# Performance work log

Measured on AMD Instinct MI355X. Metric: run time of the kernel, lower is better.

## Reference

```python
import jax, jax.numpy as jnp
import numpy as np

LN_EPS = 1e-5

def _gru_layer(x, W_ih, W_hh, b_ih, b_hh):
    # x: [B,S,Din]; W_ih: [3H,Din]; W_hh: [3H,H]; biases: [3H]
    B = x.shape[0]
    H = W_hh.shape[1]
    # Precompute input-side gate projections for all timesteps (one big GEMM).
    gx = jnp.einsum('bsd,gd->bsg', x, W_ih) + b_ih  # [B,S,3H]
    Whh_T = W_hh.T  # [H,3H]

    def step(h, gx_t):
        gh = h @ Whh_T + b_hh                     # [B,3H]
        xr, xz, xn = jnp.split(gx_t, 3, axis=-1)
        hr, hz, hn = jnp.split(gh, 3, axis=-1)
        r = jax.nn.sigmoid(xr + hr)
        z = jax.nn.sigmoid(xz + hz)
        n = jnp.tanh(xn + r * hn)
        h_new = (1.0 - z) * n + z * h
        return h_new, h_new

    h0 = jnp.zeros((B, H), dtype=x.dtype)
    h_last, ys = jax.lax.scan(step, h0, jnp.swapaxes(gx, 0, 1))  # ys: [S,B,H]
    return jnp.swapaxes(ys, 0, 1), h_last


def setup_inputs() -> dict:
    key = jax.random.key(0)
    ks = jax.random.split(key, 12)
    B, S, D, H = 256, 512, 64, 256
    L = 3
    s_in = 1.0 / np.sqrt(H)
    return {
        'x': jax.random.normal(ks[0], (B, S, D), dtype=jnp.float32),
        'W_ih0': jax.random.uniform(ks[1], (3 * H, D), jnp.float32, -s_in, s_in),
        'W_ih_rest': jax.random.uniform(ks[2], (L - 1, 3 * H, H), jnp.float32, -s_in, s_in),
        'W_hh': jax.random.uniform(ks[3], (L, 3 * H, H), jnp.float32, -s_in, s_in),
        'b_ih': jax.random.uniform(ks[4], (L, 3 * H), jnp.float32, -s_in, s_in),
        'b_hh': jax.random.uniform(ks[5], (L, 3 * H), jnp.float32, -s_in, s_in),
        'ln_gamma': jnp.ones((H,), jnp.float32),
        'ln_beta': jnp.zeros((H,), jnp.float32),
        'W1': jax.random.uniform(ks[6], (32, H), jnp.float32, -s_in, s_in),
        'b1': jax.random.uniform(ks[7], (32,), jnp.float32, -s_in, s_in),
        'W2': jax.random.uniform(ks[8], (1, 32), jnp.float32, -1 / np.sqrt(32), 1 / np.sqrt(32)),
        'b2': jax.random.uniform(ks[9], (1,), jnp.float32, -1 / np.sqrt(32), 1 / np.sqrt(32)),
    }


def reference(x, W_ih0, W_ih_rest, W_hh, b_ih, b_hh, ln_gamma, ln_beta, W1, b1, W2, b2):
    # Multi-layer GRU (batch_first), eval mode (dropout inactive).
    h = x
    L = W_hh.shape[0]
    h_last = None
    for l in range(L):
        W_ih_l = W_ih0 if l == 0 else W_ih_rest[l - 1]
        h, h_last = _gru_layer(h, W_ih_l, W_hh[l], b_ih[l], b_hh[l])
    last = h_last  # == out[:, -1, :]  [B,H]
    # LayerNorm
    mu = jnp.mean(last, axis=-1, keepdims=True)
    var = jnp.mean(jnp.square(last - mu), axis=-1, keepdims=True)
    last = (last - mu) * jax.lax.rsqrt(var + LN_EPS) * ln_gamma + ln_beta
    # MLP head
    hdn = jax.nn.relu(last @ W1.T + b1)
    pred = hdn @ W2.T + b2  # [B,1]
    return pred[:, 0]
```

## Files before the change

kernel.cpp:

```cpp
#include <hip/hip_runtime.h>
#include <stdint.h>

#define B_  256
#define S_  512
#define D_  64
#define H_  256
#define G3_ 768

typedef __attribute__((ext_vector_type(8))) short s8v;
typedef __attribute__((ext_vector_type(4))) short s4v;
typedef __attribute__((ext_vector_type(4))) float f4v;
typedef __attribute__((ext_vector_type(4))) float f4r;

#define MF(a, b, c) __builtin_amdgcn_mfma_f32_16x16x32_bf16((a), (b), (c), 0, 0, 0)

__device__ __forceinline__ unsigned short f2bf(float x) {
  unsigned u = __float_as_uint(x);
  unsigned r = (u + 0x7fffu + ((u >> 16) & 1u)) >> 16;
  return (unsigned short)r;
}
__device__ __forceinline__ float sigm(float x) {
  return __builtin_amdgcn_rcpf(1.f + __expf(-x));
}
__device__ __forceinline__ float tanh_f(float x) {
  return 1.f - 2.f * __builtin_amdgcn_rcpf(1.f + __expf(2.f * x));
}

__global__ __launch_bounds__(256) void pack_bf16(
    const float* __restrict__ src, unsigned short* __restrict__ dst, int n8)
{
  const int i = blockIdx.x * 256 + threadIdx.x;
  if (i >= n8) return;
  const float4 f0 = *(const float4*)(src + (size_t)i * 8);
  const float4 f1 = *(const float4*)(src + (size_t)i * 8 + 4);
  unsigned short h[8] = { f2bf(f0.x), f2bf(f0.y), f2bf(f0.z), f2bf(f0.w),
                          f2bf(f1.x), f2bf(f1.y), f2bf(f1.z), f2bf(f1.w) };
  *(s8v*)&dst[(size_t)i * 8] = *(s8v*)h;
}

__global__ __launch_bounds__(64) void pack_whh(
    const float* __restrict__ Whh, unsigned short* __restrict__ Whp,
    const float* __restrict__ bih, const float* __restrict__ bhh,
    float* __restrict__ bias2)
{
  const int gti = blockIdx.x, kc = blockIdx.y, lane = threadIdx.x;
  const int rowp = gti * 16 + (lane & 15);
  const int k0  = kc * 32 + (lane >> 4) * 8;
  const float* src = &Whh[(size_t)rowp * H_ + k0];
  unsigned short hi8[8];
  #pragma unroll
  for (int s = 0; s < 8; ++s) hi8[s] = f2bf(src[s]);
  const size_t o = ((size_t)(gti * 8 + kc) * 64 + lane) * 8;
  *(s8v*)&Whp[o] = *(s8v*)hi8;

  if (gti == 0 && kc == 0) {
    #pragma unroll
    for (int i = 0; i < 12; ++i) {
      int g = i * 64 + lane;
      bias2[g] = bih[g] + (g < 512 ? bhh[g] : 0.f);
    }
  }
}

__global__ __launch_bounds__(1024, 4) void fused_step(
    int s, int CH, int chsh, int cpl,
    const float* __restrict__ x, unsigned short* __restrict__ ybf,
    const unsigned short* __restrict__ wihp,
    const unsigned short* __restrict__ Whp, const float* __restrict__ bhh_all,
    const float* __restrict__ bias2, float* __restrict__ gxbase,
    float* __restrict__ hbuf)
{
  const int tid = threadIdx.x;
  const int wid = tid >> 6, lane = tid & 63;
  const int fr = lane & 15, fq = lane >> 4;
  const size_t gx_elems = (size_t)B_ * CH * G3_;

  extern __shared__ unsigned short lds_[];

  if (blockIdx.x < 48) {
    const int l = blockIdx.x >> 4;
    const int c = s - 2 * l;
    if (c < 0 || c >= cpl) return;

    const unsigned short* Whp_s = Whp + (size_t)l * G3_ * H_;
    const float* bhh_s = bhh_all + (size_t)l * G3_;
    float* hb = hbuf + (size_t)l * B_ * H_;
    const float* gx_r = gxbase + (size_t)(2 * l + (c & 1)) * gx_elems;
    const int t0s = c * CH;
    const int lastL = (l == 2) ? 1 : 0;

    unsigned short* WhN  = lds_;
    unsigned short* Abuf = lds_ + 65536;

    const int bid = blockIdx.x & 15;
    const int b0  = bid * 16;
    const int bb  = fr;

    const s8v* WhpV = (const s8v*)Whp_s;

    s8v whr[8], whz[8];
    #pragma unroll
    for (int kc = 0; kc < 8; ++kc) {
      whr[kc] = WhpV[((     wid) * 8 + kc) * 64 + lane];
      whz[kc] = WhpV[((16 + wid) * 8 + kc) * 64 + lane];
    }
    #pragma unroll
    for (int kc = 0; kc < 8; ++kc) {
      s8v v = WhpV[((32 + wid) * 8 + kc) * 64 + lane];
      *(s8v*)&WhN[(wid * 8 + kc) * 512 + lane * 8] = v;
    }

    const int u0 = 16 * wid + 4 * fq;
    const f4r bhn4 = *(const f4r*)&bhh_s[2 * H_ + u0];

    f4r hn4 = {0.f, 0.f, 0.f, 0.f};
    if (t0s != 0) hn4 = *(const f4r*)&hb[(size_t)(b0 + bb) * H_ + u0];

    const int kcw  = wid >> 1;
    const int lp   = bb | (((2 * wid + (fq >> 1)) & 3) << 4);
    const int eo   = (fq & 1) * 4;
    const int aoff = kcw * 512 + lp * 8 + eo;

    {
      s4v hh;
      #pragma unroll
      for (int j = 0; j < 4; ++j) hh[j] = (short)f2bf(hn4[j]);
      *(s4v*)&Abuf[aoff] = hh;
    }

    const float* gb0 = gx_r + ((size_t)(b0 + bb) * CH) * G3_;
    f4r xr4 = *(const f4r*)(gb0 + u0);
    f4r xz4 = *(const f4r*)(gb0 + H_ + u0);
    f4r xn4 = *(const f4r*)(gb0 + 2 * H_ + u0);

    int cur = 0;
    for (int t = 0; t < CH; ++t) {
      __syncthreads();

      const int tn = (t + 1 < CH) ? t + 1 : t;
      const float* gbn = gx_r + ((size_t)(b0 + bb) * CH + tn) * G3_;
      f4r xr_n = *(const f4r*)(gbn + u0);
      f4r xz_n = *(const f4r*)(gbn + H_ + u0);
      f4r xn_n = *(const f4r*)(gbn + 2 * H_ + u0);

      f4v accR = {}, accZ = {}, accN = {};
      #pragma unroll
      for (int kc = 0; kc < 8; ++kc) {
        s8v ahh = *(const s8v*)&Abuf[cur * 4096 + kc * 512 + lane * 8];
        s8v wn  = *(const s8v*)&WhN[(wid * 8 + kc) * 512 + lane * 8];
        accR = MF(whr[kc], ahh, accR);
        accZ = MF(whz[kc], ahh, accZ);
        accN = MF(wn,      ahh, accN);
      }

      #pragma unroll
      for (int i = 0; i < 4; ++i) {
        const float r = sigm(xr4[i] + accR[i]);
        const float z = sigm(xz4[i] + accZ[i]);
        const float n = tanh_f(xn4[i] + r * (accN[i] + bhn4[i]));
        hn4[i] = (1.f - z) * n + z * hn4[i];
      }
      s4v hh;
      #pragma unroll
      for (int j = 0; j < 4; ++j) hh[j] = (short)f2bf(hn4[j]);
      if (!lastL) {
        __builtin_nontemporal_store(
            hh, (s4v*)&ybf[((size_t)(b0 + bb) * S_ + (t0s + t)) * H_ + u0]);
      }
      *(s4v*)&Abuf[(cur ^ 1) * 4096 + aoff] = hh;
      xr4 = xr_n; xz4 = xz_n; xn4 = xn_n;
      cur ^= 1;
    }

    *(f4r*)&hb[(size_t)(b0 + bb) * H_ + u0] = hn4;

  } else {
    const int g = blockIdx.x - 48;
    const int per = CH * 12;
    const int l = g / per;
    if (l >= 3) return;
    const int c2 = s + 1 - 2 * l;
    if (c2 < 0 || c2 >= cpl) return;

    const int gidx  = g % per;
    const int mtile = gidx / 12, gtile = gidx % 12;
    const int r0 = mtile * 256, g0 = gtile * 64;

    const int    K   = (l == 0) ? D_ : H_;
    const unsigned short* Wp =
        (l == 0) ? wihp : (wihp + 49152 + (size_t)(l - 1) * 196608);
    const float* b2g = bias2 + l * 768;
    float* gx_w = gxbase + (size_t)(2 * l + (c2 & 1)) * gx_elems;
    const int t0g = c2 * CH;

    const int row = 16 * wid + fr;
    const int r = r0 + row;
    const int rg = ((r >> chsh) * S_) + t0g + (r & (CH - 1));

    const unsigned short* wp0 = Wp + (size_t)(g0 + fr) * K + fq * 8;

    f4v acc[4] = {};

    if (l == 0) {
      const float* apf = x + (size_t)rg * D_ + fq * 8;
      #pragma unroll
      for (int k0 = 0; k0 < D_; k0 += 32) {
        float4 f0 = *(const float4*)(apf + k0);
        float4 f1 = *(const float4*)(apf + k0 + 4);
        unsigned short a8[8] = { f2bf(f0.x), f2bf(f0.y), f2bf(f0.z), f2bf(f0.w),
                                 f2bf(f1.x), f2bf(f1.y), f2bf(f1.z), f2bf(f1.w) };
        s8v a = *(s8v*)a8;
        #pragma unroll
        for (int c = 0; c < 4; ++c) {
          s8v b = *(const s8v*)(wp0 + (size_t)c * 16 * K + k0);
          acc[c] = MF(a, b, acc[c]);
        }
      }
    } else {
      const unsigned short* ap = ybf + (size_t)rg * H_ + fq * 8;
      #pragma unroll
      for (int k0 = 0; k0 < H_; k0 += 32) {
        s8v a = *(const s8v*)(ap + k0);
        #pragma unroll
        for (int c = 0; c < 4; ++c) {
          s8v b = *(const s8v*)(wp0 + (size_t)c * 16 * K + k0);
          acc[c] = MF(a, b, acc[c]);
        }
      }
    }

    const int orow = r0 + wid * 16 + fq * 4;
    #pragma unroll
    for (int c = 0; c < 4; ++c) {
      const float bi = b2g[g0 + c * 16 + fr];
      #pragma unroll
      for (int i = 0; i < 4; ++i) {
        gx_w[(size_t)(orow + i) * G3_ + g0 + c * 16 + fr] = acc[c][i] + bi;
      }
    }
  }
}

__global__ __launch_bounds__(64) void head_kernel(
    const float* __restrict__ hlast, const float* __restrict__ lng,
    const float* __restrict__ lnb, const float* __restrict__ W1,
    const float* __restrict__ b1, const float* __restrict__ W2,
    const float* __restrict__ b2, float* __restrict__ out)
{
  const int b = blockIdx.x;
  const int lane = threadIdx.x;
  float4 v = *(const float4*)&hlast[(size_t)b * H_ + lane * 4];
  float s = v.x + v.y + v.z + v.w;
  #pragma unroll
  for (int m = 32; m > 0; m >>= 1) s += __shfl_xor(s, m, 64);
  const float mu = s * (1.f / 256.f);
  const float dx = v.x - mu, dy = v.y - mu, dz = v.z - mu, dw = v.w - mu;
  float q = dx*dx + dy*dy + dz*dz + dw*dw;
  #pragma unroll
  for (int m = 32; m > 0; m >>= 1) q += __shfl_xor(q, m, 64);
  const float rstd = rsqrtf(q * (1.f / 256.f) + 1e-5f);

  __shared__ float ln[256];
  const int i4 = lane * 4;
  ln[i4 + 0] = dx * rstd * lng[i4 + 0] + lnb[i4 + 0];
  ln[i4 + 1] = dy * rstd * lng[i4 + 1] + lnb[i4 + 1];
  ln[i4 + 2] = dz * rstd * lng[i4 + 2] + lnb[i4 + 2];
  ln[i4 + 3] = dw * rstd * lng[i4 + 3] + lnb[i4 + 3];
  __syncthreads();

  float hd = 0.f;
  if (lane < 32) {
    const float* w = W1 + (size_t)lane * H_;
    float a = 0.f;
    for (int k = 0; k < H_; ++k) a += ln[k] * w[k];
    a += b1[lane];
    hd = fmaxf(a, 0.f) * W2[lane];
  }
  #pragma unroll
  for (int m = 16; m > 0; m >>= 1) hd += __shfl_xor(hd, m, 64);
  if (lane == 0) out[b] = hd + b2[0];
}

extern "C" void kernel_launch(void* const* d_in, const int* in_sizes, int n_in,
                              void* d_out, int out_size, void* d_ws, size_t ws_size,
                              hipStream_t stream)
{
  const float* x     = (const float*)d_in[0];
  const float* W_ih0 = (const float*)d_in[1];
  const float* W_ihr = (const float*)d_in[2];
  const float* W_hh  = (const float*)d_in[3];
  const float* b_ih  = (const float*)d_in[4];
  const float* b_hh  = (const float*)d_in[5];
  const float* lng   = (const float*)d_in[6];
  const float* lnb   = (const float*)d_in[7];
  const float* W1    = (const float*)d_in[8];
  const float* b1    = (const float*)d_in[9];
  const float* W2    = (const float*)d_in[10];
  const float* b2    = (const float*)d_in[11];
  float* out = (float*)d_out;

  const size_t ybf_elems  = (size_t)B_ * S_ * H_;
  const size_t wihp_elems = 49152 + 2 * 196608;
  const size_t h_elems    = (size_t)B_ * H_;
  const size_t whp_elems  = (size_t)G3_ * H_;

  int CH = 32;
  while (CH > 8) {
    size_t need = ybf_elems * 2 + wihp_elems * 2
                + (6 * (size_t)B_ * CH * G3_ + 3 * h_elems + 3 * 768) * 4
                + 3 * whp_elems * 2 + 8192;
    if (need <= ws_size) break;
    CH >>= 1;
  }
  const int chsh = __builtin_ctz((unsigned)CH);
  const size_t gx_elems = (size_t)B_ * CH * G3_;
  const int cpl = S_ / CH;

  unsigned short* ybf  = (unsigned short*)d_ws;
  unsigned short* wihp = ybf + ybf_elems;
  float* gxbase = (float*)(wihp + wihp_elems);
  float* hbuf   = gxbase + 6 * gx_elems;
  unsigned short* Whp = (unsigned short*)(hbuf + 3 * h_elems);
  float* bias2 = (float*)(Whp + 3 * whp_elems);

  const size_t lds_bytes = 131072 + 16384;
  const int grid = 48 + 3 * CH * 12;

  pack_bf16<<<(49152 / 8 + 255) / 256, 256, 0, stream>>>(W_ih0, wihp, 49152 / 8);
  pack_bf16<<<(393216 / 8 + 255) / 256, 256, 0, stream>>>(
      W_ihr, wihp + 49152, 393216 / 8);
  for (int l = 0; l < 3; ++l) {
    pack_whh<<<dim3(48, 8), 64, 0, stream>>>(
        W_hh + (size_t)l * G3_ * H_, Whp + (size_t)l * whp_elems,
        b_ih + (size_t)l * G3_, b_hh + (size_t)l * G3_, bias2 + l * 768);
  }

  for (int s = -1; s <= cpl + 3; ++s) {
    fused_step<<<grid, 1024, lds_bytes, stream>>>(
        s, CH, chsh, cpl, x, ybf, wihp, Whp, b_hh, bias2, gxbase, hbuf);
  }

  head_kernel<<<256, 64, 0, stream>>>(hbuf + 2 * h_elems, lng, lnb,
                                      W1, b1, W2, b2, out);
}
```

Measured before the change: 1.739 ms.

## Store gate pre-activations in bf16 and stage input GEMM tiles through LDS

The precomputed input-gate projections (gx) are now stored and read as bf16 rather than fp32, which halves their memory traffic and footprint. That smaller footprint lets the chunk size CH grow from 32 to 64, so fewer chunked launches are needed. The input-projection GEMM blocks now stage A and W tiles through padded shared memory with coalesced loads, then write outputs through an LDS transpose as 16-byte vector stores. The cost is lower precision on gx and extra __syncthreads in the GEMM path.

```diff
diff --git a/kernel.cpp b/kernel.cpp
--- a/kernel.cpp
+++ b/kernel.cpp
@@ -18,6 +18,9 @@
   unsigned u = __float_as_uint(x);
   unsigned r = (u + 0x7fffu + ((u >> 16) & 1u)) >> 16;
   return (unsigned short)r;
+}
+__device__ __forceinline__ float bf2f(unsigned short s) {
+  return __uint_as_float(((unsigned)s) << 16);
 }
 __device__ __forceinline__ float sigm(float x) {
   return __builtin_amdgcn_rcpf(1.f + __expf(-x));
@@ -67,7 +70,7 @@
     const float* __restrict__ x, unsigned short* __restrict__ ybf,
     const unsigned short* __restrict__ wihp,
     const unsigned short* __restrict__ Whp, const float* __restrict__ bhh_all,
-    const float* __restrict__ bias2, float* __restrict__ gxbase,
+    const float* __restrict__ bias2, unsigned short* __restrict__ gxbase,
     float* __restrict__ hbuf)
 {
   const int tid = threadIdx.x;
@@ -85,7 +88,7 @@
     const unsigned short* Whp_s = Whp + (size_t)l * G3_ * H_;
     const float* bhh_s = bhh_all + (size_t)l * G3_;
     float* hb = hbuf + (size_t)l * B_ * H_;
-    const float* gx_r = gxbase + (size_t)(2 * l + (c & 1)) * gx_elems;
+    const unsigned short* gx_r = gxbase + (size_t)(2 * l + (c & 1)) * gx_elems;
     const int t0s = c * CH;
     const int lastL = (l == 2) ? 1 : 0;
 
@@ -128,20 +131,20 @@
       *(s4v*)&Abuf[aoff] = hh;
     }
 
-    const float* gb0 = gx_r + ((size_t)(b0 + bb) * CH) * G3_;
-    f4r xr4 = *(const f4r*)(gb0 + u0);
-    f4r xz4 = *(const f4r*)(gb0 + H_ + u0);
-    f4r xn4 = *(const f4r*)(gb0 + 2 * H_ + u0);
+    const unsigned short* gb0 = gx_r + ((size_t)(b0 + bb) * CH) * G3_;
+    s4v xr4 = *(const s4v*)(gb0 + u0);
+    s4v xz4 = *(const s4v*)(gb0 + H_ + u0);
+    s4v xn4 = *(const s4v*)(gb0 + 2 * H_ + u0);
 
     int cur = 0;
     for (int t = 0; t < CH; ++t) {
       __syncthreads();
 
       const int tn = (t + 1 < CH) ? t + 1 : t;
-      const float* gbn = gx_r + ((size_t)(b0 + bb) * CH + tn) * G3_;
-      f4r xr_n = *(const f4r*)(gbn + u0);
-      f4r xz_n = *(const f4r*)(gbn + H_ + u0);
-      f4r xn_n = *(const f4r*)(gbn + 2 * H_ + u0);
+      const unsigned short* gbn = gx_r + ((size_t)(b0 + bb) * CH + tn) * G3_;
+      s4v xr_n = *(const s4v*)(gbn + u0);
+      s4v xz_n = *(const s4v*)(gbn + H_ + u0);
+      s4v xn_n = *(const s4v*)(gbn + 2 * H_ + u0);
 
       f4v accR = {}, accZ = {}, accN = {};
       #pragma unroll
@@ -155,9 +158,9 @@
 
       #pragma unroll
       for (int i = 0; i < 4; ++i) {
-        const float r = sigm(xr4[i] + accR[i]);
-        const float z = sigm(xz4[i] + accZ[i]);
-        const float n = tanh_f(xn4[i] + r * (accN[i] + bhn4[i]));
+        const float r = sigm(bf2f((unsigned short)xr4[i]) + accR[i]);
+        const float z = sigm(bf2f((unsigned short)xz4[i]) + accZ[i]);
+        const float n = tanh_f(bf2f((unsigned short)xn4[i]) + r * (accN[i] + bhn4[i]));
         hn4[i] = (1.f - z) * n + z * hn4[i];
       }
       s4v hh;
@@ -190,53 +193,63 @@
     const unsigned short* Wp =
         (l == 0) ? wihp : (wihp + 49152 + (size_t)(l - 1) * 196608);
     const float* b2g = bias2 + l * 768;
-    float* gx_w = gxbase + (size_t)(2 * l + (c2 & 1)) * gx_elems;
+    unsigned short* gx_w = gxbase + (size_t)(2 * l + (c2 & 1)) * gx_elems;
     const int t0g = c2 * CH;
 
-    const int row = 16 * wid + fr;
+    unsigned short* Ah  = lds_;
+    unsigned short* Wh  = lds_ + 10240;
+    unsigned short* gxs = lds_ + 12800;
+
+    const int row = tid >> 2;
+    const int ks  = (tid & 3) * 8;
     const int r = r0 + row;
     const int rg = ((r >> chsh) * S_) + t0g + (r & (CH - 1));
 
-    const unsigned short* wp0 = Wp + (size_t)(g0 + fr) * K + fq * 8;
-
     f4v acc[4] = {};
 
-    if (l == 0) {
-      const float* apf = x + (size_t)rg * D_ + fq * 8;
-      #pragma unroll
-      for (int k0 = 0; k0 < D_; k0 += 32) {
-        float4 f0 = *(const float4*)(apf + k0);
-        float4 f1 = *(const float4*)(apf + k0 + 4);
+    for (int k0 = 0; k0 < K; k0 += 32) {
+      s8v aval;
+      if (l == 0) {
+        const float* apf = x + (size_t)rg * D_ + k0 + ks;
+        float4 f0 = *(const float4*)(apf);
+        float4 f1 = *(const float4*)(apf + 4);
         unsigned short a8[8] = { f2bf(f0.x), f2bf(f0.y), f2bf(f0.z), f2bf(f0.w),
                                  f2bf(f1.x), f2bf(f1.y), f2bf(f1.z), f2bf(f1.w) };
-        s8v a = *(s8v*)a8;
-        #pragma unroll
-        for (int c = 0; c < 4; ++c) {
-          s8v b = *(const s8v*)(wp0 + (size_t)c * 16 * K + k0);
-          acc[c] = MF(a, b, acc[c]);
-        }
-      }
-    } else {
-      const unsigned short* ap = ybf + (size_t)rg * H_ + fq * 8;
-      #pragma unroll
-      for (int k0 = 0; k0 < H_; k0 += 32) {
-        s8v a = *(const s8v*)(ap + k0);
-        #pragma unroll
-        for (int c = 0; c < 4; ++c) {
-          s8v b = *(const s8v*)(wp0 + (size_t)c * 16 * K + k0);
-          acc[c] = MF(a, b, acc[c]);
-        }
-      }
-    }
-
-    const int orow = r0 + wid * 16 + fq * 4;
+        aval = *(s8v*)a8;
+      } else {
+        aval = *(const s8v*)(ybf + (size_t)rg * H_ + k0 + ks);
+      }
+      s8v wval;
+      if (tid < 256)
+        wval = *(const s8v*)(Wp + (size_t)(g0 + row) * K + k0 + ks);
+      __syncthreads();
+      *(s8v*)&Ah[row * 40 + ks] = aval;
+      if (tid < 256) *(s8v*)&Wh[row * 40 + ks] = wval;
+      __syncthreads();
+
+      s8v a_hi = *(const s8v*)&Ah[(16 * wid + fr) * 40 + fq * 8];
+      #pragma unroll
+      for (int c = 0; c < 4; ++c) {
+        s8v b_hi = *(const s8v*)&Wh[(c * 16 + fr) * 40 + fq * 8];
+        acc[c] = MF(a_hi, b_hi, acc[c]);
+      }
+    }
+
     #pragma unroll
     for (int c = 0; c < 4; ++c) {
       const float bi = b2g[g0 + c * 16 + fr];
       #pragma unroll
-      for (int i = 0; i < 4; ++i) {
-        gx_w[(size_t)(orow + i) * G3_ + g0 + c * 16 + fr] = acc[c][i] + bi;
-      }
+      for (int i = 0; i < 4; ++i)
+        gxs[(wid * 16 + fq * 4 + i) * 64 + c * 16 + fr] = f2bf(acc[c][i] + bi);
+    }
+    __syncthreads();
+    {
+      const int srow = tid >> 2, soff = (tid & 3) * 16;
+      s8v v0 = *(const s8v*)&gxs[srow * 64 + soff];
+      s8v v1 = *(const s8v*)&gxs[srow * 64 + soff + 8];
+      unsigned short* gp = gx_w + (size_t)(r0 + srow) * G3_ + g0 + soff;
+      *(s8v*)gp = v0;
+      *(s8v*)(gp + 8) = v1;
     }
   }
 }
@@ -304,10 +317,11 @@
   const size_t h_elems    = (size_t)B_ * H_;
   const size_t whp_elems  = (size_t)G3_ * H_;
 
-  int CH = 32;
+  int CH = 64;
   while (CH > 8) {
     size_t need = ybf_elems * 2 + wihp_elems * 2
-                + (6 * (size_t)B_ * CH * G3_ + 3 * h_elems + 3 * 768) * 4
+                + 6 * (size_t)B_ * CH * G3_ * 2
+                + (3 * h_elems + 3 * 768) * 4
                 + 3 * whp_elems * 2 + 8192;
     if (need <= ws_size) break;
     CH >>= 1;
@@ -316,10 +330,10 @@
   const size_t gx_elems = (size_t)B_ * CH * G3_;
   const int cpl = S_ / CH;
 
-  unsigned short* ybf  = (unsigned short*)d_ws;
-  unsigned short* wihp = ybf + ybf_elems;
-  float* gxbase = (float*)(wihp + wihp_elems);
-  float* hbuf   = gxbase + 6 * gx_elems;
+  unsigned short* ybf    = (unsigned short*)d_ws;
+  unsigned short* wihp   = ybf + ybf_elems;
+  unsigned short* gxbase = wihp + wihp_elems;
+  float* hbuf = (float*)(gxbase + 6 * gx_elems);
   unsigned short* Whp = (unsigned short*)(hbuf + 3 * h_elems);
   float* bias2 = (float*)(Whp + 3 * whp_elems);
 
```

Measured after the change: 1.524 ms. -12.4%, faster.
